# Kernel tuning notes

Hardware: AMD Instinct MI355X
Metric: run time of the kernel (lower is better)

## Reference

```python
import jax, jax.numpy as jnp
import numpy as np

N = 6144
IN_DIM = 256
HID = 64
HEADS = 4
LAT = 32
ALPHA = 0.2  # LeakyReLU negative slope
NEG_INF = -9e15


def setup_inputs() -> dict:
    key = jax.random.key(0)
    ks = jax.random.split(key, 6)
    x = jax.random.normal(ks[0], (N, IN_DIM), jnp.float32)
    # sparse symmetric 0/1 adjacency, avg degree ~ 25
    A = (jax.random.uniform(ks[1], (N, N)) < 0.004).astype(jnp.float32)
    A = jnp.maximum(A, A.T)
    # xavier-uniform-ish params, matching pyGAT GraphAttentionLayer shapes
    s1 = float(np.sqrt(6.0 / (IN_DIM + HID)))
    W_heads = jax.random.uniform(ks[2], (HEADS, IN_DIM, HID), jnp.float32, -s1, s1)
    sa = float(np.sqrt(6.0 / (2 * HID + 1)))
    a_heads = jax.random.uniform(ks[3], (HEADS, 2 * HID), jnp.float32, -sa, sa)
    s2 = float(np.sqrt(6.0 / (HEADS * HID + LAT)))
    W_out = jax.random.uniform(ks[4], (HEADS * HID, LAT), jnp.float32, -s2, s2)
    sb = float(np.sqrt(6.0 / (2 * LAT + 1)))
    a_out = jax.random.uniform(ks[5], (2 * LAT,), jnp.float32, -sb, sb)
    return {"x": x, "A": A, "W_heads": W_heads, "a_heads": a_heads,
            "W_out": W_out, "a_out": a_out}


def _gat_layer(h, adj_mask, W, a, concat):
    # h: [N, F_in], W: [F_in, F], a: [2F]
    Wh = h @ W                              # [N, F]
    f = W.shape[1]
    e_src = Wh @ a[:f]                      # [N]
    e_dst = Wh @ a[f:]                      # [N]
    e = jax.nn.leaky_relu(e_src[:, None] + e_dst[None, :], ALPHA)  # [N, N]
    e = jnp.where(adj_mask, e, NEG_INF)
    att = jax.nn.softmax(e, axis=1)         # masked softmax over neighbors
    out = att @ Wh                          # [N, F]
    return jax.nn.elu(out) if concat else out


def reference(x, A, W_heads, a_heads, W_out, a_out):
    # normalize(A, 'sym', False): D^{-1/2} A D^{-1/2}
    deg = A.sum(axis=1)
    dinv = jnp.where(deg > 0, deg ** -0.5, 0.0)
    An = A * dinv[:, None] * dinv[None, :]
    mask = An > 0
    heads = [_gat_layer(x, mask, W_heads[i], a_heads[i], True) for i in range(HEADS)]
    h = jnp.concatenate(heads, axis=1)      # [N, HEADS*HID]
    z = jax.nn.elu(_gat_layer(h, mask, W_out, a_out, False))  # [N, LAT]
    return jax.nn.sigmoid(z @ z.T)          # [N, N]
```

## Files before the change

kernel.cpp:

```cpp
#include <hip/hip_runtime.h>
#include <hip/hip_bf16.h>

#define NN 6144
#define IN_DIM 256
#define HID 64
#define HEADS 4
#define LAT 32
#define CAP 192
#define ALPHA 0.2f
#define GEMM_BLOCKS 384

typedef __attribute__((ext_vector_type(8))) short bf16x8;
typedef __attribute__((ext_vector_type(4))) float f32x4;

__device__ __forceinline__ float elu_f(float v)   { return v > 0.f ? v : expm1f(v); }
__device__ __forceinline__ float lrelu_f(float v) { return v > 0.f ? v : ALPHA * v; }

__device__ __forceinline__ void split_bf16(float v, unsigned short& hi, unsigned short& lo) {
    unsigned u = __builtin_bit_cast(unsigned, v);
    hi = (unsigned short)(u >> 16);
    float vh = __builtin_bit_cast(float, u & 0xFFFF0000u);
    float rl = v - vh;
    lo = (unsigned short)(__builtin_bit_cast(unsigned, rl) >> 16);
}
__device__ __forceinline__ unsigned short f2bf(float f) {
    unsigned u = __builtin_bit_cast(unsigned, f);
    return (unsigned short)((u + 0x7FFFu + ((u >> 16) & 1u)) >> 16);
}
__device__ __forceinline__ float bf2f(unsigned short b) {
    return __builtin_bit_cast(float, (unsigned)b << 16);
}

__global__ __launch_bounds__(256) void k_pre(const float* __restrict__ A,
                                             const float* __restrict__ x,
                                             const float* __restrict__ Wheads,
                                             const float* __restrict__ aheads,
                                             int* __restrict__ nbr, int* __restrict__ cnt,
                                             unsigned short* __restrict__ Whb,
                                             float* __restrict__ es4, float* __restrict__ ed4) {
    __shared__ __align__(16) float smem[2048];
    int bid = blockIdx.x;
    int t = threadIdx.x;
    if (bid < GEMM_BLOCKS) {
        int head = bid & 3, m0 = (bid >> 2) * 64;
        float (*As)[64] = (float(*)[64])smem;
        float (*Bs)[64] = (float(*)[64])(smem + 1024);
        const float* Wc = Wheads + (size_t)head * IN_DIM * HID;
        int ty = t >> 4, tx = t & 15;
        float acc[4][4] = {};
        for (int k0 = 0; k0 < IN_DIM; k0 += 16) {
            {
                int row = t >> 2, k4 = (t & 3) * 4;
                float4 v = *(const float4*)(x + (size_t)(m0 + row) * IN_DIM + k0 + k4);
                As[k4 + 0][row] = v.x; As[k4 + 1][row] = v.y;
                As[k4 + 2][row] = v.z; As[k4 + 3][row] = v.w;
                int kk = t >> 4, n4 = (t & 15) * 4;
                *(float4*)&Bs[kk][n4] = *(const float4*)(Wc + (size_t)(k0 + kk) * HID + n4);
            }
            __syncthreads();
            #pragma unroll
            for (int k = 0; k < 16; ++k) {
                float4 av = *(float4*)&As[k][ty * 4];
                float4 bv = *(float4*)&Bs[k][tx * 4];
                float ar[4] = {av.x, av.y, av.z, av.w};
                float br[4] = {bv.x, bv.y, bv.z, bv.w};
                #pragma unroll
                for (int i = 0; i < 4; ++i)
                    #pragma unroll
                    for (int j = 0; j < 4; ++j)
                        acc[i][j] = fmaf(ar[i], br[j], acc[i][j]);
            }
            __syncthreads();
        }
        #pragma unroll
        for (int i = 0; i < 4; ++i) {
            ushort4 o;
            o.x = f2bf(acc[i][0]); o.y = f2bf(acc[i][1]);
            o.z = f2bf(acc[i][2]); o.w = f2bf(acc[i][3]);
            *(ushort4*)(Whb + (size_t)(m0 + ty * 4 + i) * (HEADS * HID) + head * HID + tx * 4) = o;
        }
        float4 a1v = *(const float4*)(aheads + head * 2 * HID + tx * 4);
        float4 a2v = *(const float4*)(aheads + head * 2 * HID + HID + tx * 4);
        #pragma unroll
        for (int i = 0; i < 4; ++i) {
            float p1 = acc[i][0] * a1v.x + acc[i][1] * a1v.y + acc[i][2] * a1v.z + acc[i][3] * a1v.w;
            float p2 = acc[i][0] * a2v.x + acc[i][1] * a2v.y + acc[i][2] * a2v.z + acc[i][3] * a2v.w;
            #pragma unroll
            for (int off = 8; off; off >>= 1) {
                p1 += __shfl_down(p1, off, 16);
                p2 += __shfl_down(p2, off, 16);
            }
            if (tx == 0) {
                es4[(size_t)(m0 + ty * 4 + i) * 4 + head] = p1;
                ed4[(size_t)(m0 + ty * 4 + i) * 4 + head] = p2;
            }
        }
    } else {
        int row = bid - GEMM_BLOCKS;
        int* lcnt = (int*)smem;
        const float4* Arow = (const float4*)(A + (size_t)row * NN);
        if (t == 0) *lcnt = 0;
        __syncthreads();
        int* my = nbr + (size_t)row * CAP;
        #pragma unroll
        for (int it = 0; it < NN / 4 / 256; ++it) {
            int idx4 = it * 256 + t;
            float4 v = Arow[idx4];
            int base = idx4 * 4;
            if (v.x != 0.f) { int p = atomicAdd(lcnt, 1); if (p < CAP) my[p] = base; }
            if (v.y != 0.f) { int p = atomicAdd(lcnt, 1); if (p < CAP) my[p] = base + 1; }
            if (v.z != 0.f) { int p = atomicAdd(lcnt, 1); if (p < CAP) my[p] = base + 2; }
            if (v.w != 0.f) { int p = atomicAdd(lcnt, 1); if (p < CAP) my[p] = base + 3; }
        }
        __syncthreads();
        if (t == 0) cnt[row] = *lcnt < CAP ? *lcnt : CAP;
    }
}

__global__ __launch_bounds__(256, 4) void k_attn1g2(const int* __restrict__ nbr, const int* __restrict__ cnt,
                                                    const float4* __restrict__ es4, const float4* __restrict__ ed4,
                                                    const unsigned short* __restrict__ Whb,
                                                    const float* __restrict__ Wout, const float* __restrict__ aout,
                                                    float* __restrict__ Wh2,
                                                    float* __restrict__ es2, float* __restrict__ ed2) {
    __shared__ int colS[4][CAP];
    __shared__ __align__(16) float att4[4][CAP][4];
    __shared__ __align__(16) float hrow[4][HEADS * HID];
    __shared__ __align__(16) unsigned short WoutS[IN_DIM * LAT];
    int w = threadIdx.x >> 6, l = threadIdx.x & 63;
    int i = blockIdx.x * 4 + w;
    int c = cnt[i];
    const int* nb = nbr + (size_t)i * CAP;

    #pragma unroll
    for (int it = 0; it < (IN_DIM * LAT / 4) / 256; ++it) {
        int q = it * 256 + threadIdx.x;
        float4 v = *(const float4*)(Wout + q * 4);
        ushort4 o;
        o.x = f2bf(v.x); o.y = f2bf(v.y); o.z = f2bf(v.z); o.w = f2bf(v.w);
        *(ushort4*)&WoutS[q * 4] = o;
    }
    __syncthreads();

    float4 esv = es4[i];
    float s0 = 0.f, s1 = 0.f, s2 = 0.f, s3 = 0.f;
    for (int j = l; j < c; j += 64) {
        int cj = nb[j];
        colS[w][j] = cj;
        float4 edv = ed4[cj];
        float4 e;
        e.x = __expf(lrelu_f(esv.x + edv.x));
        e.y = __expf(lrelu_f(esv.y + edv.y));
        e.z = __expf(lrelu_f(esv.z + edv.z));
        e.w = __expf(lrelu_f(esv.w + edv.w));
        *(float4*)&att4[w][j][0] = e;
        s0 += e.x; s1 += e.y; s2 += e.z; s3 += e.w;
    }
    #pragma unroll
    for (int off = 32; off; off >>= 1) {
        s0 += __shfl_down(s0, off); s1 += __shfl_down(s1, off);
        s2 += __shfl_down(s2, off); s3 += __shfl_down(s3, off);
    }
    s0 = __shfl(s0, 0); s1 = __shfl(s1, 0); s2 = __shfl(s2, 0); s3 = __shfl(s3, 0);

    int hd = l >> 4;
    float sh = hd < 2 ? (hd == 0 ? s0 : s1) : (hd == 2 ? s2 : s3);
    float invh = 1.0f / sh;
    float4 hv;
    if (c == 0) {
        float a0 = 0.f, a1 = 0.f, a2 = 0.f, a3 = 0.f;
        for (int r = 0; r < NN; ++r) {
            ushort4 v = *(const ushort4*)(Whb + (size_t)r * (HEADS * HID) + 4 * l);
            a0 += bf2f(v.x); a1 += bf2f(v.y); a2 += bf2f(v.z); a3 += bf2f(v.w);
        }
        hv.x = elu_f(a0 / NN); hv.y = elu_f(a1 / NN);
        hv.z = elu_f(a2 / NN); hv.w = elu_f(a3 / NN);
    } else {
        const unsigned short* Wb = Whb + 4 * l;
        float ax[8], ay[8], az[8], aw[8];
        #pragma unroll
        for (int k = 0; k < 8; ++k) { ax[k] = 0.f; ay[k] = 0.f; az[k] = 0.f; aw[k] = 0.f; }
        int j = 0;
        for (; j + 8 <= c; j += 8) {
            int cj[8]; float ff[8]; ushort4 vv[8];
            #pragma unroll
            for (int k = 0; k < 8; ++k) { cj[k] = colS[w][j + k]; ff[k] = att4[w][j + k][hd]; }
            #pragma unroll
            for (int k = 0; k < 8; ++k) vv[k] = *(const ushort4*)(Wb + (size_t)cj[k] * (HEADS * HID));
            #pragma unroll
            for (int k = 0; k < 8; ++k) {
                ax[k] = fmaf(ff[k], bf2f(vv[k].x), ax[k]);
                ay[k] = fmaf(ff[k], bf2f(vv[k].y), ay[k]);
                az[k] = fmaf(ff[k], bf2f(vv[k].z), az[k]);
                aw[k] = fmaf(ff[k], bf2f(vv[k].w), aw[k]);
            }
        }
        for (; j < c; ++j) {
            int cj = colS[w][j];
            float f = att4[w][j][hd];
            ushort4 v = *(const ushort4*)(Wb + (size_t)cj * (HEADS * HID));
            ax[0] = fmaf(f, bf2f(v.x), ax[0]); ay[0] = fmaf(f, bf2f(v.y), ay[0]);
            az[0] = fmaf(f, bf2f(v.z), az[0]); aw[0] = fmaf(f, bf2f(v.w), aw[0]);
        }
        float rx = ((ax[0] + ax[1]) + (ax[2] + ax[3])) + ((ax[4] + ax[5]) + (ax[6] + ax[7]));
        float ry = ((ay[0] + ay[1]) + (ay[2] + ay[3])) + ((ay[4] + ay[5]) + (ay[6] + ay[7]));
        float rz = ((az[0] + az[1]) + (az[2] + az[3])) + ((az[4] + az[5]) + (az[6] + az[7]));
        float rw = ((aw[0] + aw[1]) + (aw[2] + aw[3])) + ((aw[4] + aw[5]) + (aw[6] + aw[7]));
        hv.x = elu_f(rx * invh); hv.y = elu_f(ry * invh);
        hv.z = elu_f(rz * invh); hv.w = elu_f(rw * invh);
    }
    *(float4*)&hrow[w][4 * l] = hv;

    {
        int half = l >> 5, cc = l & 31;
        int tbase = half * 128;
        float p0 = 0.f, p1c = 0.f, p2c = 0.f, p3c = 0.f;
        #pragma unroll
        for (int tt = 0; tt < 32; ++tt) {
            p0  = fmaf(hrow[w][tbase + tt],      bf2f(WoutS[(tbase + tt) * LAT + cc]),      p0);
            p1c = fmaf(hrow[w][tbase + 32 + tt], bf2f(WoutS[(tbase + 32 + tt) * LAT + cc]), p1c);
            p2c = fmaf(hrow[w][tbase + 64 + tt], bf2f(WoutS[(tbase + 64 + tt) * LAT + cc]), p2c);
            p3c = fmaf(hrow[w][tbase + 96 + tt], bf2f(WoutS[(tbase + 96 + tt) * LAT + cc]), p3c);
        }
        float p = (p0 + p1c) + (p2c + p3c);
        p += __shfl_down(p, 32);
        if (l < 32) {
            Wh2[(size_t)i * LAT + cc] = p;
            float p1 = p * aout[cc], p2 = p * aout[LAT + cc];
            #pragma unroll
            for (int off = 16; off; off >>= 1) {
                p1 += __shfl_down(p1, off, 32);
                p2 += __shfl_down(p2, off, 32);
            }
            if (cc == 0) { es2[i] = p1; ed2[i] = p2; }
        }
    }
}

__global__ __launch_bounds__(256, 8) void k_attn2(const int* __restrict__ nbr, const int* __restrict__ cnt,
                                                  const float* __restrict__ es2, const float* __restrict__ ed2,
                                                  const float* __restrict__ Wh2,
                                                  unsigned short* __restrict__ zh, unsigned short* __restrict__ zl) {
    __shared__ float att[4][CAP];
    __shared__ int col[4][CAP];
    int w = threadIdx.x >> 6, l = threadIdx.x & 63;
    int i = blockIdx.x * 4 + w;
    int c = cnt[i];
    if (c == 0) {
        if (l < LAT) {
            float s = 0.f;
            for (int r = 0; r < NN; ++r) s += Wh2[(size_t)r * LAT + l];
            unsigned short hi, lo;
            split_bf16(elu_f(s * (1.0f / NN)), hi, lo);
            zh[(size_t)i * LAT + l] = hi;
            zl[(size_t)i * LAT + l] = lo;
        }
        return;
    }
    float esi = es2[i];
    const int* nb = nbr + (size_t)i * CAP;
    float s = 0.f;
    for (int j = l; j < c; j += 64) {
        int cj = nb[j];
        col[w][j] = cj;
        float p = __expf(lrelu_f(esi + ed2[cj]));
        att[w][j] = p;
        s += p;
    }
    #pragma unroll
    for (int off = 32; off; off >>= 1) s += __shfl_down(s, off);
    s = __shfl(s, 0);
    if (l < LAT) {
        float inv = 1.0f / s;
        float a0 = 0.f, a1 = 0.f, a2 = 0.f, a3 = 0.f;
        int j = 0;
        for (; j + 4 <= c; j += 4) {
            a0 = fmaf(att[w][j + 0], Wh2[(size_t)col[w][j + 0] * LAT + l], a0);
            a1 = fmaf(att[w][j + 1], Wh2[(size_t)col[w][j + 1] * LAT + l], a1);
            a2 = fmaf(att[w][j + 2], Wh2[(size_t)col[w][j + 2] * LAT + l], a2);
            a3 = fmaf(att[w][j + 3], Wh2[(size_t)col[w][j + 3] * LAT + l], a3);
        }
        for (; j < c; ++j)
            a0 = fmaf(att[w][j], Wh2[(size_t)col[w][j] * LAT + l], a0);
        unsigned short hi, lo;
        split_bf16(elu_f(((a0 + a1) + (a2 + a3)) * inv), hi, lo);
        zh[(size_t)i * LAT + l] = hi;
        zl[(size_t)i * LAT + l] = lo;
    }
}

__global__ __launch_bounds__(256, 8) void k_zzt(const unsigned short* __restrict__ zh,
                                                const unsigned short* __restrict__ zl,
                                                float* __restrict__ out) {
    int t = threadIdx.x, w = t >> 6, l = t & 63;
    int m0 = blockIdx.y * 64 + w * 16;
    int n0 = blockIdx.x * 64;
    int r = l & 15, kg = (l >> 4) * 8;
    bf16x8 ah = *(const bf16x8*)(zh + (size_t)(m0 + r) * LAT + kg);
    bf16x8 al = *(const bf16x8*)(zl + (size_t)(m0 + r) * LAT + kg);
    int mbase = m0 + (l >> 4) * 4;
    #pragma unroll
    for (int jp = 0; jp < 2; ++jp) {
        int nbA = n0 + (jp * 2 + 0) * 16;
        int nbB = n0 + (jp * 2 + 1) * 16;
        bf16x8 bhA = *(const bf16x8*)(zh + (size_t)(nbA + r) * LAT + kg);
        bf16x8 blA = *(const bf16x8*)(zl + (size_t)(nbA + r) * LAT + kg);
        bf16x8 bhB = *(const bf16x8*)(zh + (size_t)(nbB + r) * LAT + kg);
        bf16x8 blB = *(const bf16x8*)(zl + (size_t)(nbB + r) * LAT + kg);
        f32x4 accA = {0.f, 0.f, 0.f, 0.f};
        accA = __builtin_amdgcn_mfma_f32_16x16x32_bf16(ah, bhA, accA, 0, 0, 0);
        accA = __builtin_amdgcn_mfma_f32_16x16x32_bf16(ah, blA, accA, 0, 0, 0);
        accA = __builtin_amdgcn_mfma_f32_16x16x32_bf16(al, bhA, accA, 0, 0, 0);
        f32x4 accB = {0.f, 0.f, 0.f, 0.f};
        accB = __builtin_amdgcn_mfma_f32_16x16x32_bf16(ah, bhB, accB, 0, 0, 0);
        accB = __builtin_amdgcn_mfma_f32_16x16x32_bf16(ah, blB, accB, 0, 0, 0);
        accB = __builtin_amdgcn_mfma_f32_16x16x32_bf16(al, bhB, accB, 0, 0, 0);
        float4 oA, oB;
        oA.x = 1.0f / (1.0f + __expf(-accA[0]));
        oA.y = 1.0f / (1.0f + __expf(-accA[1]));
        oA.z = 1.0f / (1.0f + __expf(-accA[2]));
        oA.w = 1.0f / (1.0f + __expf(-accA[3]));
        oB.x = 1.0f / (1.0f + __expf(-accB[0]));
        oB.y = 1.0f / (1.0f + __expf(-accB[1]));
        oB.z = 1.0f / (1.0f + __expf(-accB[2]));
        oB.w = 1.0f / (1.0f + __expf(-accB[3]));
        *(float4*)(out + (size_t)(nbA + (l & 15)) * NN + mbase) = oA;
        *(float4*)(out + (size_t)(nbB + (l & 15)) * NN + mbase) = oB;
    }
}

extern "C" void kernel_launch(void* const* d_in, const int* in_sizes, int n_in,
                              void* d_out, int out_size, void* d_ws, size_t ws_size,
                              hipStream_t stream) {
    const float* x      = (const float*)d_in[0];
    const float* A      = (const float*)d_in[1];
    const float* Wheads = (const float*)d_in[2];
    const float* aheads = (const float*)d_in[3];
    const float* Wout   = (const float*)d_in[4];
    const float* aout   = (const float*)d_in[5];
    float* out = (float*)d_out;

    char* ws = (char*)d_ws;
    size_t o = 0;
    auto alloc = [&](size_t bytes) { void* p = ws + o; o += (bytes + 255) & ~(size_t)255; return p; };
    int*   nbr   = (int*)  alloc((size_t)NN * CAP * 4);
    int*   cnt   = (int*)  alloc((size_t)NN * 4);
    unsigned short* Whb = (unsigned short*)alloc((size_t)NN * HEADS * HID * 2);
    float* es4   = (float*)alloc((size_t)NN * 4 * 4);
    float* ed4   = (float*)alloc((size_t)NN * 4 * 4);
    float* Wh2   = (float*)alloc((size_t)NN * LAT * 4);
    float* es2   = (float*)alloc((size_t)NN * 4);
    float* ed2   = (float*)alloc((size_t)NN * 4);
    unsigned short* zh = (unsigned short*)alloc((size_t)NN * LAT * 2);
    unsigned short* zl = (unsigned short*)alloc((size_t)NN * LAT * 2);

    k_pre     <<<GEMM_BLOCKS + NN, 256, 0, stream>>>(A, x, Wheads, aheads, nbr, cnt, Whb, es4, ed4);
    k_attn1g2 <<<NN / 4, 256, 0, stream>>>(nbr, cnt, (const float4*)es4, (const float4*)ed4,
                                           Whb, Wout, aout, Wh2, es2, ed2);
    k_attn2   <<<NN / 4, 256, 0, stream>>>(nbr, cnt, es2, ed2, Wh2, zh, zl);
    k_zzt     <<<dim3(NN / 64, NN / 64), 256, 0, stream>>>(zh, zl, out);
}
```

Measured before the change: 109.2 us.

## Use MFMA for per-block Wout projection with transposed bf16 LDS layouts

Replaces the scalar FMA projection of the aggregated hidden row through Wout with bf16 MFMA 16x16x32 instructions. Wout is stored transposed with padded stride in LDS, and the four warps' rows are packed as bf16 A operands. Every warp redundantly computes the full 4-row tile and extracts its own row. Attention weights are moved to a head-major layout so the gather loop can read them with vector loads. The hidden row is now rounded to bf16 before projection, which costs some precision, and the Wout staging now uses scattered 2-byte transposed stores.

After: 108.1 us (median of 2 runs). Within noise of the previous version (-1.0%).

```diff
diff --git a/kernel.cpp b/kernel.cpp
--- a/kernel.cpp
+++ b/kernel.cpp
@@ -9,6 +9,7 @@
 #define CAP 192
 #define ALPHA 0.2f
 #define GEMM_BLOCKS 384
+#define WSTRIDE 264
 
 typedef __attribute__((ext_vector_type(8))) short bf16x8;
 typedef __attribute__((ext_vector_type(4))) float f32x4;
@@ -124,23 +125,24 @@
                                                     float* __restrict__ Wh2,
                                                     float* __restrict__ es2, float* __restrict__ ed2) {
     __shared__ int colS[4][CAP];
-    __shared__ __align__(16) float att4[4][CAP][4];
-    __shared__ __align__(16) float hrow[4][HEADS * HID];
-    __shared__ __align__(16) unsigned short WoutS[IN_DIM * LAT];
+    __shared__ __align__(16) float attH[4][HEADS][CAP];
+    __shared__ __align__(16) unsigned short hbf[4][WSTRIDE];
+    __shared__ __align__(16) unsigned short WoutT[LAT][WSTRIDE];
     int w = threadIdx.x >> 6, l = threadIdx.x & 63;
     int i = blockIdx.x * 4 + w;
     int c = cnt[i];
     const int* nb = nbr + (size_t)i * CAP;
 
     #pragma unroll
-    for (int it = 0; it < (IN_DIM * LAT / 4) / 256; ++it) {
+    for (int it = 0; it < 8; ++it) {
         int q = it * 256 + threadIdx.x;
         float4 v = *(const float4*)(Wout + q * 4);
-        ushort4 o;
-        o.x = f2bf(v.x); o.y = f2bf(v.y); o.z = f2bf(v.z); o.w = f2bf(v.w);
-        *(ushort4*)&WoutS[q * 4] = o;
-    }
-    __syncthreads();
+        int trow = q >> 3, c0 = (q * 4) & 31;
+        WoutT[c0 + 0][trow] = f2bf(v.x);
+        WoutT[c0 + 1][trow] = f2bf(v.y);
+        WoutT[c0 + 2][trow] = f2bf(v.z);
+        WoutT[c0 + 3][trow] = f2bf(v.w);
+    }
 
     float4 esv = es4[i];
     float s0 = 0.f, s1 = 0.f, s2 = 0.f, s3 = 0.f;
@@ -153,7 +155,8 @@
         e.y = __expf(lrelu_f(esv.y + edv.y));
         e.z = __expf(lrelu_f(esv.z + edv.z));
         e.w = __expf(lrelu_f(esv.w + edv.w));
-        *(float4*)&att4[w][j][0] = e;
+        attH[w][0][j] = e.x; attH[w][1][j] = e.y;
+        attH[w][2][j] = e.z; attH[w][3][j] = e.w;
         s0 += e.x; s1 += e.y; s2 += e.z; s3 += e.w;
     }
     #pragma unroll
@@ -182,9 +185,13 @@
         for (int k = 0; k < 8; ++k) { ax[k] = 0.f; ay[k] = 0.f; az[k] = 0.f; aw[k] = 0.f; }
         int j = 0;
         for (; j + 8 <= c; j += 8) {
-            int cj[8]; float ff[8]; ushort4 vv[8];
-            #pragma unroll
-            for (int k = 0; k < 8; ++k) { cj[k] = colS[w][j + k]; ff[k] = att4[w][j + k][hd]; }
+            float4 f0 = *(float4*)&attH[w][hd][j];
+            float4 f1 = *(float4*)&attH[w][hd][j + 4];
+            int4 c0v = *(int4*)&colS[w][j];
+            int4 c1v = *(int4*)&colS[w][j + 4];
+            float ff[8] = {f0.x, f0.y, f0.z, f0.w, f1.x, f1.y, f1.z, f1.w};
+            int   cj[8] = {c0v.x, c0v.y, c0v.z, c0v.w, c1v.x, c1v.y, c1v.z, c1v.w};
+            ushort4 vv[8];
             #pragma unroll
             for (int k = 0; k < 8; ++k) vv[k] = *(const ushort4*)(Wb + (size_t)cj[k] * (HEADS * HID));
             #pragma unroll
@@ -197,7 +204,7 @@
         }
         for (; j < c; ++j) {
             int cj = colS[w][j];
-            float f = att4[w][j][hd];
+            float f = attH[w][hd][j];
             ushort4 v = *(const ushort4*)(Wb + (size_t)cj * (HEADS * HID));
             ax[0] = fmaf(f, bf2f(v.x), ax[0]); ay[0] = fmaf(f, bf2f(v.y), ay[0]);
             az[0] = fmaf(f, bf2f(v.z), az[0]); aw[0] = fmaf(f, bf2f(v.w), aw[0]);
@@ -209,30 +216,39 @@
         hv.x = elu_f(rx * invh); hv.y = elu_f(ry * invh);
         hv.z = elu_f(rz * invh); hv.w = elu_f(rw * invh);
     }
-    *(float4*)&hrow[w][4 * l] = hv;
-
     {
-        int half = l >> 5, cc = l & 31;
-        int tbase = half * 128;
-        float p0 = 0.f, p1c = 0.f, p2c = 0.f, p3c = 0.f;
-        #pragma unroll
-        for (int tt = 0; tt < 32; ++tt) {
-            p0  = fmaf(hrow[w][tbase + tt],      bf2f(WoutS[(tbase + tt) * LAT + cc]),      p0);
-            p1c = fmaf(hrow[w][tbase + 32 + tt], bf2f(WoutS[(tbase + 32 + tt) * LAT + cc]), p1c);
-            p2c = fmaf(hrow[w][tbase + 64 + tt], bf2f(WoutS[(tbase + 64 + tt) * LAT + cc]), p2c);
-            p3c = fmaf(hrow[w][tbase + 96 + tt], bf2f(WoutS[(tbase + 96 + tt) * LAT + cc]), p3c);
-        }
-        float p = (p0 + p1c) + (p2c + p3c);
-        p += __shfl_down(p, 32);
-        if (l < 32) {
-            Wh2[(size_t)i * LAT + cc] = p;
-            float p1 = p * aout[cc], p2 = p * aout[LAT + cc];
-            #pragma unroll
-            for (int off = 16; off; off >>= 1) {
-                p1 += __shfl_down(p1, off, 32);
-                p2 += __shfl_down(p2, off, 32);
-            }
-            if (cc == 0) { es2[i] = p1; ed2[i] = p2; }
+        ushort4 o;
+        o.x = f2bf(hv.x); o.y = f2bf(hv.y); o.z = f2bf(hv.z); o.w = f2bf(hv.w);
+        *(ushort4*)&hbf[w][4 * l] = o;
+    }
+    __syncthreads();
+
+    {
+        int r = l & 15, kg = l >> 4;
+        f32x4 accA = {0.f, 0.f, 0.f, 0.f};
+        f32x4 accB = {0.f, 0.f, 0.f, 0.f};
+        #pragma unroll
+        for (int k0 = 0; k0 < 8; ++k0) {
+            bf16x8 af = {0, 0, 0, 0, 0, 0, 0, 0};
+            if (r < 4) af = *(const bf16x8*)&hbf[r][k0 * 32 + kg * 8];
+            bf16x8 b0 = *(const bf16x8*)&WoutT[r][k0 * 32 + kg * 8];
+            bf16x8 b1 = *(const bf16x8*)&WoutT[16 + r][k0 * 32 + kg * 8];
+            accA = __builtin_amdgcn_mfma_f32_16x16x32_bf16(af, b0, accA, 0, 0, 0);
+            accB = __builtin_amdgcn_mfma_f32_16x16x32_bf16(af, b1, accB, 0, 0, 0);
+        }
+        float v0 = (w == 0) ? accA[0] : (w == 1) ? accA[1] : (w == 2) ? accA[2] : accA[3];
+        float v1 = (w == 0) ? accB[0] : (w == 1) ? accB[1] : (w == 2) ? accB[2] : accB[3];
+        if (l < 16) {
+            Wh2[(size_t)i * LAT + l]      = v0;
+            Wh2[(size_t)i * LAT + 16 + l] = v1;
+            float p1 = v0 * aout[l] + v1 * aout[16 + l];
+            float p2 = v0 * aout[32 + l] + v1 * aout[48 + l];
+            #pragma unroll
+            for (int off = 8; off; off >>= 1) {
+                p1 += __shfl_down(p1, off, 16);
+                p2 += __shfl_down(p2, off, 16);
+            }
+            if (l == 0) { es2[i] = p1; ed2[i] = p2; }
         }
     }
 }
```
